# Kernel tuning notes

Measured on AMD Instinct MI355X. Metric: run time of the kernel, lower is better.

The kernel has to match this reference:

```python
import jax, jax.numpy as jnp
import numpy as np

B, N, D = 2, 2048, 256
H = 8
HD = D // H
SCALE = HD ** 0.5  # NOTE: source MULTIPLIES by sqrt(head_dim)
EPS = 1e-5
DFF = 4 * D


def setup_inputs() -> dict:
    key = jax.random.key(0)
    ks = jax.random.split(key, 9)
    s = lambda fan_in: 1.0 / np.sqrt(fan_in)
    return {
        "x": jax.random.normal(ks[0], (B, N, D), dtype=jnp.float32),
        # weights stored [in, out] (transposed torch Linear)
        "qkv_w": jax.random.normal(ks[1], (D, 3 * D), dtype=jnp.float32) * s(D),
        "proj_w": jax.random.normal(ks[2], (D, D), dtype=jnp.float32) * s(D),
        "proj_b": jax.random.normal(ks[3], (D,), dtype=jnp.float32) * 0.01,
        "fc1_w": jax.random.normal(ks[4], (D, DFF), dtype=jnp.float32) * s(D),
        "fc1_b": jax.random.normal(ks[5], (DFF,), dtype=jnp.float32) * 0.01,
        "fc2_w": jax.random.normal(ks[6], (DFF, D), dtype=jnp.float32) * s(DFF),
        "fc2_b": jax.random.normal(ks[7], (D,), dtype=jnp.float32) * 0.01,
        "ln1_g": jnp.ones((D,), dtype=jnp.float32),
        "ln1_b": jnp.zeros((D,), dtype=jnp.float32),
    }


def _layernorm(x, g, b):
    mu = jnp.mean(x, axis=-1, keepdims=True)
    var = jnp.mean(jnp.square(x - mu), axis=-1, keepdims=True)
    return (x - mu) * jax.lax.rsqrt(var + EPS) * g + b


def reference(x, qkv_w, proj_w, proj_b, fc1_w, fc1_b, fc2_w, fc2_b, ln1_g, ln1_b):
    b, n, d = x.shape
    # --- MHA ---
    qkv = (x @ qkv_w).reshape(b, n, 3, H, HD)
    q = qkv[:, :, 0].transpose(0, 2, 1, 3)  # [B,H,N,HD]
    k = qkv[:, :, 1].transpose(0, 2, 1, 3)
    v = qkv[:, :, 2].transpose(0, 2, 1, 3)
    att = jnp.einsum("bhqd,bhkd->bhqk", q, k) * SCALE  # multiplied, per source
    att = jax.nn.softmax(att, axis=-1)
    out = jnp.einsum("bhqk,bhkd->bhqd", att, v)
    out = out.transpose(0, 2, 1, 3).reshape(b, n, d)
    out = out @ proj_w + proj_b
    # --- post-norm residual ---
    net = _layernorm(out + x, ln1_g, ln1_b)
    shortcut = net
    # --- MLP (NO activation in source forward) ---
    net = (net @ fc1_w + fc1_b) @ fc2_w + fc2_b
    return net + shortcut
```

## Files before the change

kernel.cpp:

```cpp
#include <hip/hip_runtime.h>


typedef __attribute__((ext_vector_type(8))) short short8;
typedef __attribute__((ext_vector_type(8))) _Float16 half8;
typedef __attribute__((ext_vector_type(4))) _Float16 half4;
typedef __attribute__((ext_vector_type(2))) __fp16 fp16x2;
typedef __attribute__((ext_vector_type(4))) float floatx4;
typedef __attribute__((ext_vector_type(2))) unsigned int uint2v;
typedef unsigned short u16;

#define MFMAG(a,b,c)  __builtin_amdgcn_mfma_f32_16x16x32_f16((a),(b),(c),0,0,0)
#if __has_builtin(__builtin_amdgcn_mfma_f32_16x16x16_f16)
#define MFMAPV(a,b,c) __builtin_amdgcn_mfma_f32_16x16x16_f16((a),(b),(c),0,0,0)
#else
#define MFMAPV(a,b,c) __builtin_amdgcn_mfma_f32_16x16x16f16((a),(b),(c),0,0,0)
#endif
#define CLF 8.1615404f

#if __has_builtin(__builtin_amdgcn_exp2f)
#define EX2(x) __builtin_amdgcn_exp2f(x)
#else
#define EX2(x) exp2f(x)
#endif

__device__ __forceinline__ float bf2f(u16 u) { return __uint_as_float(((unsigned)u) << 16); }
__device__ __forceinline__ float h2f(u16 u) { _Float16 h = *(_Float16*)&u; return (float)h; }
__device__ __forceinline__ u16 f2h(float f) { _Float16 h = (_Float16)f; return *(u16*)&h; }
__device__ __forceinline__ unsigned pkh2(float a, float b) {
#if __has_builtin(__builtin_amdgcn_cvt_pkrtz)
  fp16x2 h = __builtin_amdgcn_cvt_pkrtz(a, b);
  return *(unsigned*)&h;
#else
  return (unsigned)f2h(a) | ((unsigned)f2h(b) << 16);
#endif
}
__device__ __forceinline__ void gll16(const void* g, void* l) {
  __builtin_amdgcn_global_load_lds((const __attribute__((address_space(1))) void*)g,
                                   (__attribute__((address_space(3))) void*)l, 16, 0, 0);
}

__global__ __launch_bounds__(256) void prep_k(
    const void* __restrict__ x, const void* __restrict__ qkv_w,
    const void* __restrict__ proj_w, const void* __restrict__ fc1_w,
    const void* __restrict__ fc2_w, const void* __restrict__ proj_b,
    const void* __restrict__ fc1_b, const void* __restrict__ fc2_b,
    const void* __restrict__ ln_g, const void* __restrict__ ln_b,
    u16* __restrict__ x_f, u16* __restrict__ wq_f,
    u16* __restrict__ wt_proj, u16* __restrict__ wt_fc1, u16* __restrict__ wt_fc2,
    u16* __restrict__ b_proj, u16* __restrict__ b_fc1, u16* __restrict__ b_fc2,
    u16* __restrict__ g_ln, u16* __restrict__ bb_ln)
{
  const int lane = threadIdx.x & 63;
  const float probe = bf2f(((const u16*)qkv_w)[lane]);
  const bool f32 = __ballot(!(fabsf(probe) < 1000.0f)) != 0ull;
  const int bid = blockIdx.x, tid = threadIdx.x;
  #define RD(p, i) (f32 ? ((const float*)(p))[i] : bf2f(((const u16*)(p))[i]))
  if (bid < 4096) {
    const size_t i = (size_t)bid * 256 + tid;
    x_f[i] = f2h(RD(x, i));
  } else if (bid < 4864) {
    const int idx = (bid - 4096) * 256 + tid;
    const int n = idx >> 8, k = idx & 255;
    wq_f[idx] = f2h(RD(qkv_w, (size_t)k * 768 + n));
  } else if (bid < 5120) {
    const int idx = (bid - 4864) * 256 + tid;
    wt_proj[idx] = f2h(RD(proj_w, (size_t)(idx & 255) * 256 + (idx >> 8)));
  } else if (bid < 6144) {
    const int idx = (bid - 5120) * 256 + tid;
    wt_fc1[idx] = f2h(RD(fc1_w, (size_t)(idx & 255) * 1024 + (idx >> 8)));
  } else if (bid < 7168) {
    const int idx = (bid - 6144) * 256 + tid;
    wt_fc2[idx] = f2h(RD(fc2_w, (size_t)(idx & 1023) * 256 + (idx >> 10)));
  } else {
    const int j = (bid - 7168) * 256 + tid;
    if (j < 256)       b_proj[j]        = f2h(RD(proj_b, j));
    else if (j < 1280) b_fc1[j - 256]   = f2h(RD(fc1_b, j - 256));
    else if (j < 1536) b_fc2[j - 1280]  = f2h(RD(fc2_b, j - 1280));
    else if (j < 1792) g_ln[j - 1536]   = f2h(RD(ln_g, j - 1536));
    else               bb_ln[j - 1792]  = f2h(RD(ln_b, j - 1792));
  }
  #undef RD
}

template<int TW, int EPI, bool BIAS, bool RES, bool COMB>
__global__ __launch_bounds__(256) void gemm_k(
    const u16* __restrict__ A, const u16* __restrict__ Bt, const u16* __restrict__ A2,
    const u16* __restrict__ bias, const u16* __restrict__ res,
    void* __restrict__ out0, u16* __restrict__ aux1, u16* __restrict__ aux3,
    const float* __restrict__ muc,
    int M, int Nn, int K)
{
  constexpr int BT = TW * 32;
  constexpr int NC = TW / 2;
  __shared__ __align__(16) u16 As[BT][40];
  __shared__ __align__(16) u16 Bs[BT][40];
  __shared__ __align__(16) u16 Vt[(EPI == 2) ? 64 * 72 : 1];
  const int tid = threadIdx.x;
  const int m0 = blockIdx.y * BT, n0 = blockIdx.x * BT;
  const int wid = tid >> 6, lane = tid & 63;
  const int wm = (wid >> 1) * (TW * 16), wn = (wid & 1) * (TW * 16);
  const int lm = lane & 15, quad = lane >> 4;

  floatx4 zero = {0.f, 0.f, 0.f, 0.f};
  floatx4 acc[TW][TW];
#pragma unroll
  for (int i = 0; i < TW; ++i)
#pragma unroll
    for (int j = 0; j < TW; ++j) acc[i][j] = zero;

  auto comb8 = [&](int t, int col8) -> short8 {
    const size_t o = (size_t)t * 256 + col8;
    const int h = col8 >> 5;
    const float m0_ = muc[t * 8 + h],          m1_ = muc[32768 + t * 8 + h];
    const float m2_ = muc[65536 + t * 8 + h],  m3_ = muc[98304 + t * 8 + h];
    const float M = fmaxf(fmaxf(m0_, m1_), fmaxf(m2_, m3_));
    float w0 = EX2(m0_ - M), w1 = EX2(m1_ - M), w2 = EX2(m2_ - M), w3 = EX2(m3_ - M);
    const float inv = 1.f / (w0 + w1 + w2 + w3);
    w0 *= inv; w1 *= inv; w2 *= inv; w3 *= inv;
    short8 a0 = *(const short8*)&A[o],  a1 = *(const short8*)&A[o + 1048576];
    short8 a2 = *(const short8*)&A2[o], a3 = *(const short8*)&A2[o + 1048576];
    float v[8];
#pragma unroll
    for (int j = 0; j < 8; ++j)
      v[j] = w0 * h2f((u16)a0[j]) + w1 * h2f((u16)a1[j])
           + w2 * h2f((u16)a2[j]) + w3 * h2f((u16)a3[j]);
    uint2v uu0 = {pkh2(v[0], v[1]), pkh2(v[2], v[3])};
    uint2v uu1 = {pkh2(v[4], v[5]), pkh2(v[6], v[7])};
    short8 r;
    *(uint2v*)&r = uu0; *((uint2v*)&r + 1) = uu1;
    return r;
  };

  int srow[NC], soff[NC];
#pragma unroll
  for (int c = 0; c < NC; ++c) {
    const int cid = tid * NC + c;
    srow[c] = cid >> 2; soff[c] = (cid & 3) * 8;
  }
  short8 ra[NC], rb[NC];
#pragma unroll
  for (int c = 0; c < NC; ++c) {
    rb[c] = *(const short8*)&Bt[(size_t)(n0 + srow[c]) * K + soff[c]];
    if (COMB) ra[c] = comb8(m0 + srow[c], soff[c]);
    else      ra[c] = *(const short8*)&A[(size_t)(m0 + srow[c]) * K + soff[c]];
  }
  for (int k0 = 0; k0 < K; k0 += 32) {
    if (k0) __syncthreads();
#pragma unroll
    for (int c = 0; c < NC; ++c) {
      *(short8*)&As[srow[c]][soff[c]] = ra[c];
      *(short8*)&Bs[srow[c]][soff[c]] = rb[c];
    }
    __syncthreads();
    if (k0 + 32 < K) {
#pragma unroll
      for (int c = 0; c < NC; ++c) {
        rb[c] = *(const short8*)&Bt[(size_t)(n0 + srow[c]) * K + k0 + 32 + soff[c]];
        if (COMB) ra[c] = comb8(m0 + srow[c], k0 + 32 + soff[c]);
        else      ra[c] = *(const short8*)&A[(size_t)(m0 + srow[c]) * K + k0 + 32 + soff[c]];
      }
    }
    half8 fa[TW], fb[TW];
#pragma unroll
    for (int t = 0; t < TW; ++t) {
      fa[t] = *(const half8*)&As[wm + t * 16 + lm][quad * 8];
      fb[t] = *(const half8*)&Bs[wn + t * 16 + lm][quad * 8];
    }
#pragma unroll
    for (int i = 0; i < TW; ++i)
#pragma unroll
      for (int j = 0; j < TW; ++j)
        acc[i][j] = MFMAG(fa[i], fb[j], acc[i][j]);
  }

  if (EPI == 2 && n0 >= 512) {
    __syncthreads();
#pragma unroll
    for (int i = 0; i < TW; ++i)
#pragma unroll
      for (int j = 0; j < TW; ++j)
#pragma unroll
        for (int r = 0; r < 4; ++r)
          Vt[(wn + j * 16 + lm) * 72 + wm + i * 16 + quad * 4 + r] = f2h(acc[i][j][r]);
    __syncthreads();
    const int bb = m0 >> 11, n = m0 & 2047;
#pragma unroll
    for (int pass = 0; pass < 2; ++pass) {
      const int dl = (tid >> 3) + pass * 32;
      const int oct = tid & 7;
      const int col = n0 - 512 + dl;
      const int d = col & 31, hh = col >> 5;
      short8 v = *(const short8*)&Vt[dl * 72 + oct * 8];
      *(short8*)&((u16*)out0)[(size_t)((bb * 8 + hh) * 32 + d) * 2048 + n + oct * 8] = v;
    }
    return;
  }

#pragma unroll
  for (int i = 0; i < TW; ++i) {
    const int rowb = m0 + wm + i * 16 + quad * 4;
#pragma unroll
    for (int j = 0; j < TW; ++j) {
      const int col = n0 + wn + j * 16 + lm;
      const float bv = BIAS ? h2f(bias[col]) : 0.f;
#pragma unroll
      for (int r = 0; r < 4; ++r) {
        const int row = rowb + r;
        float v = acc[i][j][r] + bv;
        const size_t o = (size_t)row * Nn + col;
        if (RES) v += h2f(res[o]);
        if (EPI == 0) {
          ((float*)out0)[o] = v;
        } else if (EPI == 1) {
          ((u16*)out0)[o] = f2h(v);
        } else {
          if (col < 256) aux1[(size_t)row * 256 + col] = f2h(v);
          else           aux3[(size_t)row * 256 + (col - 256)] = f2h(v);
        }
      }
    }
  }
}

__global__ __launch_bounds__(256) void projln_k(
    const u16* __restrict__ A,
    const u16* __restrict__ A2,
    const u16* __restrict__ Bt,
    const u16* __restrict__ bias,
    const u16* xh,
    const u16* __restrict__ g, const u16* __restrict__ bb,
    const float* __restrict__ muc,
    u16* net)
{
  __shared__ __align__(16) u16 As[16][40];
  __shared__ __align__(16) u16 Bs[256][40];
  __shared__ float ss[4][16], ssq[4][16];
  const int tid = threadIdx.x;
  const int m0 = blockIdx.x * 16;
  const int wid = tid >> 6, lane = tid & 63;
  const int lm = lane & 15, quad = lane >> 4;

  floatx4 zero = {0.f, 0.f, 0.f, 0.f};
  floatx4 acc[4] = {zero, zero, zero, zero};

  auto comb8 = [&](int t, int col8) -> short8 {
    const size_t o = (size_t)t * 256 + col8;
    const int h = col8 >> 5;
    const float m0_ = muc[t * 8 + h],          m1_ = muc[32768 + t * 8 + h];
    const float m2_ = muc[65536 + t * 8 + h],  m3_ = muc[98304 + t * 8 + h];
    const float M = fmaxf(fmaxf(m0_, m1_), fmaxf(m2_, m3_));
    float w0 = EX2(m0_ - M), w1 = EX2(m1_ - M), w2 = EX2(m2_ - M), w3 = EX2(m3_ - M);
    const float inv = 1.f / (w0 + w1 + w2 + w3);
    w0 *= inv; w1 *= inv; w2 *= inv; w3 *= inv;
    short8 a0 = *(const short8*)&A[o],  a1 = *(const short8*)&A[o + 1048576];
    short8 a2 = *(const short8*)&A2[o], a3 = *(const short8*)&A2[o + 1048576];
    float v[8];
#pragma unroll
    for (int j = 0; j < 8; ++j)
      v[j] = w0 * h2f((u16)a0[j]) + w1 * h2f((u16)a1[j])
           + w2 * h2f((u16)a2[j]) + w3 * h2f((u16)a3[j]);
    uint2v uu0 = {pkh2(v[0], v[1]), pkh2(v[2], v[3])};
    uint2v uu1 = {pkh2(v[4], v[5]), pkh2(v[6], v[7])};
    short8 r;
    *(uint2v*)&r = uu0; *((uint2v*)&r + 1) = uu1;
    return r;
  };

  const int arow = lane >> 2, aoff = (lane & 3) * 8;
  int browv[4];
#pragma unroll
  for (int c = 0; c < 4; ++c) browv[c] = wid * 64 + c * 16 + (lane >> 2);
  const int boff = (lane & 3) * 8;

  short8 ra; short8 rb[4];
  if (wid == 0) ra = comb8(m0 + arow, aoff);
#pragma unroll
  for (int c = 0; c < 4; ++c)
    rb[c] = *(const short8*)&Bt[(size_t)browv[c] * 256 + boff];

  for (int k0 = 0; k0 < 256; k0 += 32) {
    if (k0) __syncthreads();
    if (wid == 0) *(short8*)&As[arow][aoff] = ra;
#pragma unroll
    for (int c = 0; c < 4; ++c)
      *(short8*)&Bs[browv[c]][boff] = rb[c];
    __syncthreads();
    if (k0 + 32 < 256) {
      if (wid == 0) ra = comb8(m0 + arow, k0 + 32 + aoff);
#pragma unroll
      for (int c = 0; c < 4; ++c)
        rb[c] = *(const short8*)&Bt[(size_t)browv[c] * 256 + k0 + 32 + boff];
    }
    half8 fa = *(const half8*)&As[lm][quad * 8];
    half8 fb[4];
#pragma unroll
    for (int j = 0; j < 4; ++j)
      fb[j] = *(const half8*)&Bs[wid * 64 + j * 16 + lm][quad * 8];
#pragma unroll
    for (int j = 0; j < 4; ++j)
      acc[j] = MFMAG(fa, fb[j], acc[j]);
  }

  const int colb = wid * 64 + lm;
  float s[4] = {0.f, 0.f, 0.f, 0.f}, sq[4] = {0.f, 0.f, 0.f, 0.f};
  float vout[4][4];
#pragma unroll
  for (int j = 0; j < 4; ++j) {
    const int col = colb + j * 16;
    const float bv = h2f(bias[col]);
#pragma unroll
    for (int r = 0; r < 4; ++r) {
      const int row = quad * 4 + r;
      float v = acc[j][r] + bv + h2f(xh[(size_t)(m0 + row) * 256 + col]);
      vout[j][r] = v;
      s[r] += v; sq[r] += v * v;
    }
  }
#pragma unroll
  for (int d = 1; d < 16; d <<= 1)
#pragma unroll
    for (int r = 0; r < 4; ++r) {
      s[r] += __shfl_xor(s[r], d);
      sq[r] += __shfl_xor(sq[r], d);
    }
  if (lm == 0)
#pragma unroll
    for (int r = 0; r < 4; ++r) { ss[wid][quad * 4 + r] = s[r]; ssq[wid][quad * 4 + r] = sq[r]; }
  __syncthreads();
#pragma unroll
  for (int r = 0; r < 4; ++r) {
    const int row = quad * 4 + r;
    const float ts = ss[0][row] + ss[1][row] + ss[2][row] + ss[3][row];
    const float tq = ssq[0][row] + ssq[1][row] + ssq[2][row] + ssq[3][row];
    const float mean = ts * (1.f / 256.f);
    const float var = tq * (1.f / 256.f) - mean * mean;
    const float is = rsqrtf(var + 1e-5f);
#pragma unroll
    for (int j = 0; j < 4; ++j) {
      const int col = colb + j * 16;
      net[(size_t)(m0 + row) * 256 + col] =
          f2h((vout[j][r] - mean) * is * h2f(g[col]) + h2f(bb[col]));
    }
  }
}

template<int CHUNKS>
__global__ __launch_bounds__(256) void attn_k(
    const u16* __restrict__ qf16, const u16* __restrict__ kf16,
    const u16* __restrict__ vt, u16* __restrict__ outp, u16* __restrict__ out23,
    float* __restrict__ mu)
{
  __shared__ __align__(16) u16 Ks[2][64][32];
  __shared__ __align__(16) u16 Vs[2][32][64];
  const int tid = threadIdx.x, wid = tid >> 6, lane = tid & 63;
  const int lm = lane & 15, quad = lane >> 4;
  const int bid = blockIdx.x;
  const int chunk = (CHUNKS > 1) ? (bid >> 9) : 0;
  const int qblk = bid & 31, bh = (bid >> 5) & 15;
  const int b = bh >> 3, h = bh & 7;
  const int q0 = qblk * 64 + wid * 16;
  const size_t tb = (size_t)b * 2048;
  const int NT = 32 / CHUNKS;
  const int kofs = chunk * (2048 / CHUNKS);

  half8 qh;
  { size_t off = (tb + q0 + lm) * 256 + h * 32 + quad * 8;
    qh = *(const half8*)&qf16[off]; }

  const int kkey = tid >> 2, kg = tid & 3;
  const size_t kb = (tb + kofs + kkey) * 256 + h * 32 + kg * 8;
  const int vd = tid >> 3, vp = tid & 7, vk8 = vp ^ (vd & 7);
  const size_t vb = (size_t)(bh * 32 + vd) * 2048 + kofs + vk8 * 8;

  gll16(kf16 + kb, (u16*)Ks + tid * 8);
  gll16(vt  + vb,  (u16*)Vs + tid * 8);

  float mrun = -1e30f, lrun = 0.f;
  floatx4 o0 = {0.f,0.f,0.f,0.f}, o1 = {0.f,0.f,0.f,0.f};

  for (int kt = 0; kt < NT; ++kt) {
    const int buf = kt & 1;
    __syncthreads();
    if (kt < NT - 1) {
      const int nb = (buf ^ 1) * 2048;
      const size_t ko = (size_t)(kt + 1) * 16384;
      const size_t vo = (size_t)(kt + 1) * 64;
      gll16(kf16 + kb + ko, (u16*)Ks + nb + tid * 8);
      gll16(vt  + vb + vo,  (u16*)Vs + nb + tid * 8);
    }

    floatx4 z[4];
#pragma unroll
    for (int kf = 0; kf < 4; ++kf) {
      half8 khf = *(const half8*)&Ks[buf][kf * 16 + lm][quad * 8];
      floatx4 zz = {0.f,0.f,0.f,0.f};
      z[kf] = MFMAG(khf, qh, zz);
    }
    float zm = fmaxf(fmaxf(fmaxf(z[0][0], z[0][1]), fmaxf(z[0][2], z[0][3])),
               fmaxf(fmaxf(z[1][0], z[1][1]), fmaxf(z[1][2], z[1][3])));
    zm = fmaxf(zm, fmaxf(fmaxf(fmaxf(z[2][0], z[2][1]), fmaxf(z[2][2], z[2][3])),
                   fmaxf(fmaxf(z[3][0], z[3][1]), fmaxf(z[3][2], z[3][3]))));
    zm = fmaxf(zm, __shfl_xor(zm, 16));
    zm = fmaxf(zm, __shfl_xor(zm, 32));
    const float mn = fmaxf(mrun, zm);
    const float alpha = EX2((mrun - mn) * CLF);
    const float mc = mn * CLF;
    mrun = mn;
    float ls = 0.f;
    half4 pb[4];
#pragma unroll
    for (int kf = 0; kf < 4; ++kf) {
      const float p0 = EX2(__builtin_fmaf(z[kf][0], CLF, -mc));
      const float p1 = EX2(__builtin_fmaf(z[kf][1], CLF, -mc));
      const float p2 = EX2(__builtin_fmaf(z[kf][2], CLF, -mc));
      const float p3 = EX2(__builtin_fmaf(z[kf][3], CLF, -mc));
      ls += (p0 + p1) + (p2 + p3);
      uint2v uu = {pkh2(p0, p1), pkh2(p2, p3)};
      pb[kf] = *(half4*)&uu;
    }
    ls += __shfl_xor(ls, 16);
    ls += __shfl_xor(ls, 32);
    lrun = lrun * alpha + ls;
#pragma unroll
    for (int r = 0; r < 4; ++r) { o0[r] *= alpha; o1[r] *= alpha; }
    const u16* vbase = (const u16*)Vs + buf * 2048;
#pragma unroll
    for (int kf = 0; kf < 4; ++kf) {
      const int k8 = 2 * kf + (quad >> 1);
      const int d0 = lm, d1 = 16 + lm;
      half4 vf0 = *(const half4*)(vbase + (d0 * 8 + (k8 ^ (d0 & 7))) * 8 + (quad & 1) * 4);
      half4 vf1 = *(const half4*)(vbase + (d1 * 8 + (k8 ^ (d1 & 7))) * 8 + (quad & 1) * 4);
      o0 = MFMAPV(vf0, pb[kf], o0);
      o1 = MFMAPV(vf1, pb[kf], o1);
    }
  }
  const float inv = 1.0f / lrun;
  const size_t tok = tb + q0 + lm;
  u16* dst = ((CHUNKS > 2 && chunk >= 2) ? out23 : outp) + (size_t)(chunk & 1) * 1048576;
  const size_t rowo = tok * 256 + h * 32;
#pragma unroll
  for (int r = 0; r < 4; ++r) {
    dst[rowo + quad * 4 + r]      = f2h(o0[r] * inv);
    dst[rowo + 16 + quad * 4 + r] = f2h(o1[r] * inv);
  }
  if (CHUNKS > 1 && quad == 0)
    mu[chunk * 32768 + tok * 8 + h] = __builtin_fmaf(mrun, CLF, __log2f(lrun));
}

template<int CHUNKS>
__global__ __launch_bounds__(256) void combine_k(u16* __restrict__ d,
                                                 const u16* __restrict__ e,
                                                 const float* __restrict__ mu)
{
  const int t = blockIdx.x, c = threadIdx.x, h = c >> 5;
  const size_t o = (size_t)t * 256 + c;
  float m[CHUNKS];
  float M = -1e30f;
#pragma unroll
  for (int i = 0; i < CHUNKS; ++i) { m[i] = mu[i * 32768 + t * 8 + h]; M = fmaxf(M, m[i]); }
  float wsum = 0.f, acc = 0.f;
#pragma unroll
  for (int i = 0; i < CHUNKS; ++i) {
    const float w = EX2(m[i] - M);
    const u16 v = (i < 2) ? d[o + (size_t)i * 1048576] : e[o + (size_t)(i - 2) * 1048576];
    wsum += w; acc += w * h2f(v);
  }
  d[o] = f2h(acc / wsum);
}

__global__ __launch_bounds__(256) void ln_k(const float* __restrict__ pf,
                                            const u16* __restrict__ xh,
                                            const u16* __restrict__ g,
                                            const u16* __restrict__ bta,
                                            u16* __restrict__ net)
{
  const int t = blockIdx.x, c = threadIdx.x;
  const size_t o = (size_t)t * 256 + c;
  float v = pf[o] + h2f(xh[o]);
  float s = v, s2 = v * v;
#pragma unroll
  for (int d = 1; d < 64; d <<= 1) { s += __shfl_xor(s, d); s2 += __shfl_xor(s2, d); }
  __shared__ float ss[4], ss2[4];
  const int w = c >> 6;
  if ((c & 63) == 0) { ss[w] = s; ss2[w] = s2; }
  __syncthreads();
  s = ss[0] + ss[1] + ss[2] + ss[3];
  s2 = ss2[0] + ss2[1] + ss2[2] + ss2[3];
  const float mu = s * (1.f / 256.f);
  const float var = s2 * (1.f / 256.f) - mu * mu;
  const float is = rsqrtf(var + 1e-5f);
  net[o] = f2h((v - mu) * is * h2f(g[c]) + h2f(bta[c]));
}

extern "C" void kernel_launch(void* const* d_in, const int* in_sizes, int n_in,
                              void* d_out, int out_size, void* d_ws, size_t ws_size,
                              hipStream_t stream) {
  const void* x      = d_in[0];
  const void* qkv_w  = d_in[1];
  const void* proj_w = d_in[2];
  const void* proj_b = d_in[3];
  const void* fc1_w  = d_in[4];
  const void* fc1_b  = d_in[5];
  const void* fc2_w  = d_in[6];
  const void* fc2_b  = d_in[7];
  const void* ln_g   = d_in[8];
  const void* ln_b   = d_in[9];

  char* ws = (char*)d_ws;
  u16* b_proj  = (u16*)(ws + 4096);
  u16* b_fc1   = (u16*)(ws + 8192);
  u16* b_fc2   = (u16*)(ws + 12288);
  u16* g_ln    = (u16*)(ws + 16384);
  u16* bb_ln   = (u16*)(ws + 20480);
  u16* wq_f    = (u16*)(ws + 131072);
  u16* wt_proj = (u16*)(ws + 524288);
  u16* wt_fc1  = (u16*)(ws + 655360);
  u16* wt_fc2  = (u16*)(ws + 1179648);
  u16* x_f     = (u16*)(ws + 2097152);
  u16* q_f16   = (u16*)(ws + 4194304);
  u16* k_f16   = (u16*)(ws + 6291456);
  u16* vt      = (u16*)(ws + 8388608);
  float* mu    = (float*)(ws + 10485760);
  u16* out23   = (u16*)(ws + 11010048);
  u16* attn    = (u16*)d_out;

  u16* net4    = x_f;
  u16* hbuf4   = (u16*)(ws + 4194304);

  float* projf = (float*)(ws + 4194304);
  u16* net     = (u16*)(ws + 11010048);
  u16* hbuf    = (u16*)(ws + 2097152);

  const bool sk4 = ws_size >= 15204352;
  const bool sk2 = ws_size >= 11010048;

  prep_k<<<7176, 256, 0, stream>>>(x, qkv_w, proj_w, fc1_w, fc2_w,
                                   proj_b, fc1_b, fc2_b, ln_g, ln_b,
                                   x_f, wq_f, wt_proj, wt_fc1, wt_fc2,
                                   b_proj, b_fc1, b_fc2, g_ln, bb_ln);

  gemm_k<2, 2, false, false, false><<<dim3(12, 64), 256, 0, stream>>>(
      x_f, wq_f, nullptr, nullptr, nullptr, vt, q_f16, k_f16, nullptr, 4096, 768, 256);
  if (sk4) {
    attn_k<4><<<2048, 256, 0, stream>>>(q_f16, k_f16, vt, attn, out23, mu);
    projln_k<<<256, 256, 0, stream>>>(attn, out23, wt_proj, b_proj, x_f,
                                      g_ln, bb_ln, mu, net4);
    gemm_k<2, 1, true, false, false><<<dim3(16, 64), 256, 0, stream>>>(
        net4, wt_fc1, nullptr, b_fc1, nullptr, hbuf4, nullptr, nullptr, nullptr,
        4096, 1024, 256);
    gemm_k<2, 0, true, true, false><<<dim3(4, 64), 256, 0, stream>>>(
        hbuf4, wt_fc2, nullptr, b_fc2, net4, d_out, nullptr, nullptr, nullptr,
        4096, 256, 1024);
    return;
  }
  if (sk2) {
    attn_k<2><<<1024, 256, 0, stream>>>(q_f16, k_f16, vt, attn, nullptr, mu);
    combine_k<2><<<4096, 256, 0, stream>>>(attn, nullptr, mu);
    gemm_k<2, 0, true, false, false><<<dim3(4, 64), 256, 0, stream>>>(
        attn, wt_proj, nullptr, b_proj, nullptr, projf, nullptr, nullptr, nullptr,
        4096, 256, 256);
  } else {
    attn_k<1><<<512, 256, 0, stream>>>(q_f16, k_f16, vt, attn, nullptr, nullptr);
    gemm_k<2, 0, true, false, false><<<dim3(4, 64), 256, 0, stream>>>(
        attn, wt_proj, nullptr, b_proj, nullptr, projf, nullptr, nullptr, nullptr,
        4096, 256, 256);
  }
  ln_k<<<4096, 256, 0, stream>>>(projf, x_f, g_ln, bb_ln, net);
  gemm_k<2, 1, true, false, false><<<dim3(16, 64), 256, 0, stream>>>(
      net, wt_fc1, nullptr, b_fc1, nullptr, hbuf, nullptr, nullptr, nullptr,
      4096, 1024, 256);
  gemm_k<2, 0, true, true, false><<<dim3(4, 64), 256, 0, stream>>>(
      hbuf, wt_fc2, nullptr, b_fc2, net, d_out, nullptr, nullptr, nullptr,
      4096, 256, 1024);
}
```

Before: 143.8 us.

## Tile weight transposes through LDS and double-prefetch fc2 GEMM loads

The weight-transpose part of the prep kernel now has each block transpose a 64x64 tile through shared memory. Both the global reads and writes are coalesced, where before every output element was a strided gather, and the grid shrinks accordingly. Separately, the fc2 GEMM (K=1024) gets a two-deep register prefetch so global loads are issued two K-steps ahead, hiding more latency. The cost is more registers per thread in fc2 and an LDS tile plus a barrier in prep.

```diff
diff --git a/kernel.cpp b/kernel.cpp
--- a/kernel.cpp
+++ b/kernel.cpp
@@ -50,6 +50,7 @@
     u16* __restrict__ b_proj, u16* __restrict__ b_fc1, u16* __restrict__ b_fc2,
     u16* __restrict__ g_ln, u16* __restrict__ bb_ln)
 {
+  __shared__ u16 tr[64][70];
   const int lane = threadIdx.x & 63;
   const float probe = bf2f(((const u16*)qkv_w)[lane]);
   const bool f32 = __ballot(!(fabsf(probe) < 1000.0f)) != 0ull;
@@ -58,31 +59,42 @@
   if (bid < 4096) {
     const size_t i = (size_t)bid * 256 + tid;
     x_f[i] = f2h(RD(x, i));
-  } else if (bid < 4864) {
-    const int idx = (bid - 4096) * 256 + tid;
-    const int n = idx >> 8, k = idx & 255;
-    wq_f[idx] = f2h(RD(qkv_w, (size_t)k * 768 + n));
-  } else if (bid < 5120) {
-    const int idx = (bid - 4864) * 256 + tid;
-    wt_proj[idx] = f2h(RD(proj_w, (size_t)(idx & 255) * 256 + (idx >> 8)));
-  } else if (bid < 6144) {
-    const int idx = (bid - 5120) * 256 + tid;
-    wt_fc1[idx] = f2h(RD(fc1_w, (size_t)(idx & 255) * 1024 + (idx >> 8)));
-  } else if (bid < 7168) {
-    const int idx = (bid - 6144) * 256 + tid;
-    wt_fc2[idx] = f2h(RD(fc2_w, (size_t)(idx & 1023) * 256 + (idx >> 10)));
+  } else if (bid < 4288) {
+    int idx = bid - 4096;
+    const void* src; u16* dst; int Ns, Kt, tk, tn;
+    if (idx < 48)       { src = qkv_w;  dst = wq_f;    Ns = 768;  Kt = 256;
+                          tk = idx & 3;  tn = idx >> 2; }
+    else if (idx < 64)  { idx -= 48;  src = proj_w; dst = wt_proj; Ns = 256; Kt = 256;
+                          tk = idx & 3;  tn = idx >> 2; }
+    else if (idx < 128) { idx -= 64;  src = fc1_w;  dst = wt_fc1;  Ns = 1024; Kt = 256;
+                          tk = idx & 3;  tn = idx >> 2; }
+    else                { idx -= 128; src = fc2_w;  dst = wt_fc2;  Ns = 256;  Kt = 1024;
+                          tk = idx & 15; tn = idx >> 4; }
+    const int k0 = tk * 64, n0 = tn * 64;
+    const int r = tid >> 6, c = tid & 63;
+#pragma unroll
+    for (int p = 0; p < 16; ++p) {
+      const int k = k0 + p * 4 + r;
+      tr[c][p * 4 + r] = f2h(RD(src, (size_t)k * Ns + n0 + c));
+    }
+    __syncthreads();
+#pragma unroll
+    for (int p = 0; p < 16; ++p) {
+      const int n = n0 + p * 4 + r;
+      dst[(size_t)n * Kt + k0 + c] = tr[p * 4 + r][c];
+    }
   } else {
-    const int j = (bid - 7168) * 256 + tid;
+    const int j = (bid - 4288) * 256 + tid;
     if (j < 256)       b_proj[j]        = f2h(RD(proj_b, j));
     else if (j < 1280) b_fc1[j - 256]   = f2h(RD(fc1_b, j - 256));
     else if (j < 1536) b_fc2[j - 1280]  = f2h(RD(fc2_b, j - 1280));
     else if (j < 1792) g_ln[j - 1536]   = f2h(RD(ln_g, j - 1536));
-    else               bb_ln[j - 1792]  = f2h(RD(ln_b, j - 1792));
+    else if (j < 2048) bb_ln[j - 1792]  = f2h(RD(ln_b, j - 1792));
   }
   #undef RD
 }
 
-template<int TW, int EPI, bool BIAS, bool RES, bool COMB>
+template<int TW, int EPI, bool BIAS, bool RES, bool COMB, bool PF2 = false>
 __global__ __launch_bounds__(256) void gemm_k(
     const u16* __restrict__ A, const u16* __restrict__ Bt, const u16* __restrict__ A2,
     const u16* __restrict__ bias, const u16* __restrict__ res,
@@ -137,27 +149,38 @@
     const int cid = tid * NC + c;
     srow[c] = cid >> 2; soff[c] = (cid & 3) * 8;
   }
-  short8 ra[NC], rb[NC];
+  short8 ra[PF2 ? 2 : 1][NC], rb[PF2 ? 2 : 1][NC];
 #pragma unroll
   for (int c = 0; c < NC; ++c) {
-    rb[c] = *(const short8*)&Bt[(size_t)(n0 + srow[c]) * K + soff[c]];
-    if (COMB) ra[c] = comb8(m0 + srow[c], soff[c]);
-    else      ra[c] = *(const short8*)&A[(size_t)(m0 + srow[c]) * K + soff[c]];
-  }
-  for (int k0 = 0; k0 < K; k0 += 32) {
+    rb[0][c] = *(const short8*)&Bt[(size_t)(n0 + srow[c]) * K + soff[c]];
+    if (COMB) ra[0][c] = comb8(m0 + srow[c], soff[c]);
+    else      ra[0][c] = *(const short8*)&A[(size_t)(m0 + srow[c]) * K + soff[c]];
+  }
+  if (PF2 && K > 32) {
+#pragma unroll
+    for (int c = 0; c < NC; ++c) {
+      rb[1][c] = *(const short8*)&Bt[(size_t)(n0 + srow[c]) * K + 32 + soff[c]];
+      if (COMB) ra[1][c] = comb8(m0 + srow[c], 32 + soff[c]);
+      else      ra[1][c] = *(const short8*)&A[(size_t)(m0 + srow[c]) * K + 32 + soff[c]];
+    }
+  }
+  int it = 0;
+  for (int k0 = 0; k0 < K; k0 += 32, ++it) {
+    const int cur = PF2 ? (it & 1) : 0;
     if (k0) __syncthreads();
 #pragma unroll
     for (int c = 0; c < NC; ++c) {
-      *(short8*)&As[srow[c]][soff[c]] = ra[c];
-      *(short8*)&Bs[srow[c]][soff[c]] = rb[c];
+      *(short8*)&As[srow[c]][soff[c]] = ra[cur][c];
+      *(short8*)&Bs[srow[c]][soff[c]] = rb[cur][c];
     }
     __syncthreads();
-    if (k0 + 32 < K) {
+    const int kn = k0 + (PF2 ? 64 : 32);
+    if (kn < K) {
 #pragma unroll
       for (int c = 0; c < NC; ++c) {
-        rb[c] = *(const short8*)&Bt[(size_t)(n0 + srow[c]) * K + k0 + 32 + soff[c]];
-        if (COMB) ra[c] = comb8(m0 + srow[c], k0 + 32 + soff[c]);
-        else      ra[c] = *(const short8*)&A[(size_t)(m0 + srow[c]) * K + k0 + 32 + soff[c]];
+        rb[cur][c] = *(const short8*)&Bt[(size_t)(n0 + srow[c]) * K + kn + soff[c]];
+        if (COMB) ra[cur][c] = comb8(m0 + srow[c], kn + soff[c]);
+        else      ra[cur][c] = *(const short8*)&A[(size_t)(m0 + srow[c]) * K + kn + soff[c]];
       }
     }
     half8 fa[TW], fb[TW];
@@ -534,7 +557,7 @@
   const bool sk4 = ws_size >= 15204352;
   const bool sk2 = ws_size >= 11010048;
 
-  prep_k<<<7176, 256, 0, stream>>>(x, qkv_w, proj_w, fc1_w, fc2_w,
+  prep_k<<<4296, 256, 0, stream>>>(x, qkv_w, proj_w, fc1_w, fc2_w,
                                    proj_b, fc1_b, fc2_b, ln_g, ln_b,
                                    x_f, wq_f, wt_proj, wt_fc1, wt_fc2,
                                    b_proj, b_fc1, b_fc2, g_ln, bb_ln);
@@ -548,7 +571,7 @@
     gemm_k<2, 1, true, false, false><<<dim3(16, 64), 256, 0, stream>>>(
         net4, wt_fc1, nullptr, b_fc1, nullptr, hbuf4, nullptr, nullptr, nullptr,
         4096, 1024, 256);
-    gemm_k<2, 0, true, true, false><<<dim3(4, 64), 256, 0, stream>>>(
+    gemm_k<2, 0, true, true, false, true><<<dim3(4, 64), 256, 0, stream>>>(
         hbuf4, wt_fc2, nullptr, b_fc2, net4, d_out, nullptr, nullptr, nullptr,
         4096, 256, 1024);
     return;
```

New measurement: 200.6 us. +39.5%, slower.
